# Performance work log

Measured on AMD Instinct MI355X. Metric: run time of the kernel, lower is better.

The kernel has to match this reference:

```python
import jax, jax.numpy as jnp
import numpy as np

B, T, D, H = 2, 2048, 2048, 16
HD = D // H  # 128


def _rope_tables(t, hd):
    # standard RoPE frequencies
    inv_freq = 1.0 / (10000.0 ** (np.arange(0, hd, 2, dtype=np.float32) / hd))
    pos = np.arange(t, dtype=np.float32)
    freqs = np.outer(pos, inv_freq)          # [t, hd/2]
    emb = np.concatenate([freqs, freqs], -1)  # [t, hd]
    return jnp.asarray(np.cos(emb)), jnp.asarray(np.sin(emb))


def setup_inputs() -> dict:
    key = jax.random.key(0)
    k1, k2, k3 = jax.random.split(key, 3)
    x = jax.random.normal(k1, (B, T, D), dtype=jnp.float32)
    cos, sin = _rope_tables(T, HD)
    Wqkv = jax.random.normal(k2, (3 * D, D), dtype=jnp.float32) * (D ** -0.5)
    Wout = jax.random.normal(k3, (D, D), dtype=jnp.float32) * (D ** -0.5)
    return {"x": x, "cos": cos, "sin": sin, "Wqkv": Wqkv, "Wout": Wout}


def _rotate_half(u):
    u1, u2 = jnp.split(u, 2, axis=-1)
    return jnp.concatenate([-u2, u1], axis=-1)


def _apply_rotary(u, cos, sin):
    # u: [b,h,t,hd]; cos/sin: [t,hd] broadcast over b,h
    return u * cos[None, None] + _rotate_half(u) * sin[None, None]


def reference(x, cos, sin, Wqkv, Wout):
    b, t, d = x.shape
    qkv = jnp.einsum('btd,ed->bte', x, Wqkv)                 # [b,t,3d]
    qkv = qkv.reshape(b, t, 3, H, HD).transpose(2, 0, 3, 1, 4)  # [3,b,h,t,hd]
    q, k, v = qkv[0], qkv[1], qkv[2]
    q = _apply_rotary(q, cos, sin)
    k = _apply_rotary(k, cos, sin)
    scale = 1.0 / jnp.sqrt(jnp.asarray(HD, dtype=x.dtype))
    scores = jnp.einsum('bhqe,bhke->bhqk', q, k) * scale      # [b,h,t,t]
    causal = jnp.tril(jnp.ones((t, t), dtype=bool))
    scores = jnp.where(causal[None, None], scores, jnp.asarray(-jnp.inf, dtype=scores.dtype))
    probs = jax.nn.softmax(scores, axis=-1)
    attn = jnp.einsum('bhqk,bhke->bhqe', probs, v)            # [b,h,t,hd]
    attn = attn.transpose(0, 2, 1, 3).reshape(b, t, d)
    return jnp.einsum('btd,ed->bte', attn, Wout)
```

## Files before the change

kernel.cpp:

```cpp
#include <hip/hip_runtime.h>
#include <hip/hip_bf16.h>
#include <stdint.h>

#define T_SEQ 2048
#define D_MODEL 2048
#define N_HEADS 16
#define HEAD_DIM 128

typedef __hip_bfloat16 bf16_t;
typedef __attribute__((ext_vector_type(8))) short short8;
typedef __attribute__((ext_vector_type(4))) short short4v;
typedef __attribute__((ext_vector_type(4))) float f32x4;
typedef __attribute__((ext_vector_type(16))) float f32x16;

__device__ __forceinline__ unsigned short f2bf(float x) {
  union { float f; unsigned u; } c; c.f = x;
  unsigned u = c.u;
  u += 0x7fffu + ((u >> 16) & 1u);
  return (unsigned short)(u >> 16);
}
__device__ __forceinline__ float bf2f(short v) {
  union { unsigned u; float f; } c;
  c.u = ((unsigned)(unsigned short)v) << 16;
  return c.f;
}
__device__ __forceinline__ void async16(const bf16_t* g, bf16_t* l) {
  __builtin_amdgcn_global_load_lds(
      (const __attribute__((address_space(1))) void*)g,
      (__attribute__((address_space(3))) void*)l, 16, 0, 0);
}

__global__ __launch_bounds__(256) void cvt3_kernel(
    const float* __restrict__ x, const float* __restrict__ wqkv,
    const float* __restrict__ wout,
    unsigned short* __restrict__ xb, unsigned short* __restrict__ wqkvb,
    unsigned short* __restrict__ woutb) {
  const int N1 = 4096 * 2048 / 4;
  const int N2 = 6144 * 2048 / 4;
  const int N3 = 2048 * 2048 / 4;
  const int total = N1 + N2 + N3;
  for (int i = blockIdx.x * 256 + threadIdx.x; i < total; i += gridDim.x * 256) {
    const float* src; unsigned short* dst; int j;
    if (i < N1)            { src = x;    dst = xb;    j = i; }
    else if (i < N1 + N2)  { src = wqkv; dst = wqkvb; j = i - N1; }
    else                   { src = wout; dst = woutb; j = i - N1 - N2; }
    float4 v = ((const float4*)src)[j];
    short4v o;
    o[0] = (short)f2bf(v.x); o[1] = (short)f2bf(v.y);
    o[2] = (short)f2bf(v.z); o[3] = (short)f2bf(v.w);
    ((short4v*)dst)[j] = o;
  }
}

template<int F32OUT>
__global__ __launch_bounds__(512, 4) void gemm_tp_kernel(
    const bf16_t* __restrict__ A, const bf16_t* __restrict__ Bm,
    float* __restrict__ Cf, unsigned short* __restrict__ Cb,
    int M, int N, int K, int nbn) {
  __shared__ bf16_t lds[36864];
  const int tid = threadIdx.x;
  const int w = tid >> 6, lane = tid & 63;
  const int wm = w >> 2, wn = w & 3;
  const int l15 = lane & 15, g = lane >> 4;

  const int nwg = gridDim.x;
  const int cpx = nwg >> 3;
  const int wg = (blockIdx.x & 7) * cpx + (blockIdx.x >> 3);
  const int bm0 = (wg / nbn) * 128, bn0 = (wg % nbn) * 256;

  const int sl = tid >> 3;
  const int su = (tid & 7) ^ (sl & 7);
  const int srow = (sl << 1) | (su >> 2);
  const int sc8 = su & 3;
  const bf16_t* agA = A + (size_t)(bm0 + srow) * K + sc8 * 8;
  const bf16_t* agB = Bm + (size_t)(bn0 + srow) * K + sc8 * 8;

#define STAGE(KT, SB) do {                                                    \
    bf16_t* _d = lds + (SB) * 12288 + w * 512;                                \
    async16(agA + (size_t)(KT) * 32, _d);                                     \
    async16(agB + (size_t)(KT) * 32, _d + 4096);                              \
    async16(agB + 128 * (size_t)K + (size_t)(KT) * 32, _d + 8192);            \
  } while (0)

  const int lhalf = l15 >> 1;
  const int aoff = lhalf * 64 + (((((l15 & 1) << 2) | g) ^ lhalf)) * 8;
  const bf16_t* Abase = lds + wm * 2048 + aoff;
  const bf16_t* Bbase = lds + 4096 + wn * 2048 + aoff;

  f32x4 acc[4][4];
#pragma unroll
  for (int i = 0; i < 4; ++i)
#pragma unroll
    for (int j = 0; j < 4; ++j)
#pragma unroll
      for (int e = 0; e < 4; ++e) acc[i][j][e] = 0.0f;

  STAGE(0, 0);
  STAGE(1, 1);

  const int NT = K >> 5;
  int cb = 0, sb = 2;
  for (int kt = 0; kt < NT - 1; ++kt) {
    asm volatile("s_waitcnt vmcnt(3)" ::: "memory");
    __builtin_amdgcn_s_barrier();
    const bf16_t* Ab = Abase + cb * 12288;
    const bf16_t* Bb = Bbase + cb * 12288;
    short8 af[4], bfr[4];
#pragma unroll
    for (int mi = 0; mi < 4; ++mi) af[mi] = *(const short8*)(Ab + mi * 512);
#pragma unroll
    for (int ni = 0; ni < 4; ++ni) bfr[ni] = *(const short8*)(Bb + ni * 512);
    if (kt < NT - 2) STAGE(kt + 2, sb);
    __builtin_amdgcn_s_setprio(1);
#pragma unroll
    for (int mi = 0; mi < 4; ++mi)
#pragma unroll
      for (int ni = 0; ni < 4; ++ni)
        acc[mi][ni] = __builtin_amdgcn_mfma_f32_16x16x32_bf16(
            af[mi], bfr[ni], acc[mi][ni], 0, 0, 0);
    __builtin_amdgcn_s_setprio(0);
    cb = (cb == 2) ? 0 : cb + 1;
    sb = (sb == 2) ? 0 : sb + 1;
  }
  {
    asm volatile("s_waitcnt vmcnt(0)" ::: "memory");
    __builtin_amdgcn_s_barrier();
    const bf16_t* Ab = Abase + cb * 12288;
    const bf16_t* Bb = Bbase + cb * 12288;
    short8 af[4], bfr[4];
#pragma unroll
    for (int mi = 0; mi < 4; ++mi) af[mi] = *(const short8*)(Ab + mi * 512);
#pragma unroll
    for (int ni = 0; ni < 4; ++ni) bfr[ni] = *(const short8*)(Bb + ni * 512);
    __builtin_amdgcn_s_setprio(1);
#pragma unroll
    for (int mi = 0; mi < 4; ++mi)
#pragma unroll
      for (int ni = 0; ni < 4; ++ni)
        acc[mi][ni] = __builtin_amdgcn_mfma_f32_16x16x32_bf16(
            af[mi], bfr[ni], acc[mi][ni], 0, 0, 0);
    __builtin_amdgcn_s_setprio(0);
  }
#undef STAGE

#pragma unroll
  for (int mi = 0; mi < 4; ++mi)
#pragma unroll
    for (int ni = 0; ni < 4; ++ni)
#pragma unroll
      for (int r = 0; r < 4; ++r) {
        int mr = bm0 + wm * 64 + mi * 16 + g * 4 + r;
        int nc = bn0 + wn * 64 + ni * 16 + l15;
        if (F32OUT)
          Cf[(size_t)mr * N + nc] = acc[mi][ni][r];
        else
          Cb[(size_t)mr * N + nc] = f2bf(acc[mi][ni][r]);
      }
}

__global__ __launch_bounds__(256) void rope_kernel(
    const bf16_t* __restrict__ qkv,
    const float* __restrict__ cosb, const float* __restrict__ sinb,
    bf16_t* __restrict__ qo, bf16_t* __restrict__ ko, bf16_t* __restrict__ vT) {
  const int nTT = T_SEQ / 64;
  const int bx = blockIdx.x;
  const int bh = bx / nTT, tt = bx % nTT;
  const int b = bh / N_HEADS, h = bh % N_HEADS;
  const int tid = threadIdx.x;
  __shared__ bf16_t vlds[64][136];

  const float SC = 0.08838834764831845f;

#pragma unroll
  for (int it = 0; it < 2; ++it) {
    int item = it * 256 + tid;
    int r = item >> 3, cg = item & 7;
    int t = tt * 64 + r;
    int c0 = cg * 8;
    size_t base = ((size_t)b * T_SEQ + t) * (size_t)(3 * D_MODEL) + (size_t)h * HEAD_DIM;

    float cs0[8], sn0[8], cs1[8], sn1[8];
    {
      const float* cp = cosb + (size_t)t * HEAD_DIM + c0;
      const float* sp = sinb + (size_t)t * HEAD_DIM + c0;
      float4 a0 = *(const float4*)(cp), a1 = *(const float4*)(cp + 4);
      float4 b0 = *(const float4*)(cp + 64), b1 = *(const float4*)(cp + 68);
      float4 s0 = *(const float4*)(sp), s1 = *(const float4*)(sp + 4);
      float4 t0 = *(const float4*)(sp + 64), t1 = *(const float4*)(sp + 68);
      cs0[0]=a0.x; cs0[1]=a0.y; cs0[2]=a0.z; cs0[3]=a0.w; cs0[4]=a1.x; cs0[5]=a1.y; cs0[6]=a1.z; cs0[7]=a1.w;
      cs1[0]=b0.x; cs1[1]=b0.y; cs1[2]=b0.z; cs1[3]=b0.w; cs1[4]=b1.x; cs1[5]=b1.y; cs1[6]=b1.z; cs1[7]=b1.w;
      sn0[0]=s0.x; sn0[1]=s0.y; sn0[2]=s0.z; sn0[3]=s0.w; sn0[4]=s1.x; sn0[5]=s1.y; sn0[6]=s1.z; sn0[7]=s1.w;
      sn1[0]=t0.x; sn1[1]=t0.y; sn1[2]=t0.z; sn1[3]=t0.w; sn1[4]=t1.x; sn1[5]=t1.y; sn1[6]=t1.z; sn1[7]=t1.w;
    }

#pragma unroll
    for (int sec = 0; sec < 2; ++sec) {
      size_t sbase = base + (size_t)sec * D_MODEL;
      short8 lo = *(const short8*)(qkv + sbase + c0);
      short8 hi = *(const short8*)(qkv + sbase + 64 + c0);
      short8 olo, ohi;
#pragma unroll
      for (int e = 0; e < 8; ++e) {
        float xl = bf2f(lo[e]), xh = bf2f(hi[e]);
        float rl = xl * cs0[e] - xh * sn0[e];
        float rh = xh * cs1[e] + xl * sn1[e];
        if (sec == 0) { rl *= SC; rh *= SC; }
        olo[e] = (short)f2bf(rl);
        ohi[e] = (short)f2bf(rh);
      }
      bf16_t* dst = (sec == 0 ? qo : ko) + ((size_t)bh * T_SEQ + t) * HEAD_DIM + c0;
      *(short8*)dst = olo;
      *(short8*)(dst + 64) = ohi;
    }

    short8 v0 = *(const short8*)(qkv + base + 2 * D_MODEL + c0);
    short8 v1 = *(const short8*)(qkv + base + 2 * D_MODEL + 64 + c0);
    *(short8*)&vlds[r][c0] = v0;
    *(short8*)&vlds[r][64 + c0] = v1;
  }
  __syncthreads();

  int hd = tid >> 1, hf = tid & 1;
  bf16_t* dst = vT + ((size_t)bh * HEAD_DIM + hd) * T_SEQ + tt * 64 + hf * 32;
#pragma unroll
  for (int jj = 0; jj < 4; ++jj) {
    short8 o;
#pragma unroll
    for (int e = 0; e < 8; ++e)
      o[e] = *(const short*)&vlds[hf * 32 + jj * 8 + e][hd];
    *(short8*)(dst + jj * 8) = o;
  }
}

__global__ __launch_bounds__(256, 2) void attn_kernel(
    const bf16_t* __restrict__ q, const bf16_t* __restrict__ k,
    const bf16_t* __restrict__ vT, unsigned short* __restrict__ attn) {
  const int bx = blockIdx.x;
  const int bh = bx & 31;
  const int qi = (bx >> 5) & 7;
  const int qt = (bx >> 8) ? qi : 15 - qi;
  const int b = bh / N_HEADS, h = bh % N_HEADS;
  const int tid = threadIdx.x;
  const int w = tid >> 6, lane = tid & 63;
  const int l31 = lane & 31, hi = lane >> 5;
  const int swz = l31 & 7;
  const float LOG2E = 1.44269504088896340736f;

  __shared__ bf16_t smem[32768];

  const bf16_t* qb = q + (size_t)bh * T_SEQ * HEAD_DIM;
  const bf16_t* kb = k + (size_t)bh * T_SEQ * HEAD_DIM;
  const bf16_t* vb = vT + (size_t)bh * HEAD_DIM * T_SEQ;

  const int qlo = qt * 128 + w * 32;
  const int qhi = qlo + 31;
  const int qrow = qlo + l31;

  short8 qf[8];
#pragma unroll
  for (int ks = 0; ks < 8; ++ks)
    qf[ks] = *(const short8*)(qb + (size_t)qrow * HEAD_DIM + ks * 16 + hi * 8);

  float m = -3.0e38f, l = 0.0f;
  f32x16 O[4];
#pragma unroll
  for (int dt = 0; dt < 4; ++dt)
#pragma unroll
    for (int r = 0; r < 16; ++r) O[dt][r] = 0.0f;

#define STAGE_TILES(KT, BU) {                                                    \
    _Pragma("unroll")                                                            \
    for (int j = 0; j < 4; ++j) {                                                \
      int s = j * 4 + w;                                                         \
      int row = s * 4 + (lane >> 4);                                             \
      int gc = (lane & 15) ^ (row & 7);                                          \
      async16(kb + (size_t)((KT) * 64 + row) * HEAD_DIM + gc * 8,                \
              smem + (BU) * 8192 + s * 512);                                     \
    }                                                                            \
    _Pragma("unroll")                                                            \
    for (int j = 0; j < 4; ++j) {                                                \
      int s = j * 4 + w;                                                         \
      int row = s * 8 + (lane >> 3);                                             \
      int gc = (lane & 7) ^ (row & 7);                                           \
      async16(vb + (size_t)row * T_SEQ + (KT) * 64 + gc * 8,                     \
              smem + 16384 + (BU) * 8192 + s * 512);                             \
    }                                                                            \
  }

  STAGE_TILES(0, 0);
  __syncthreads();
  int buf = 0;

  const int lastk = 2 * qt + 1;
  for (int kt = 0; kt <= lastk; ++kt) {
    if (kt < lastk) STAGE_TILES(kt + 1, buf ^ 1);
    const bf16_t* Ks = smem + buf * 8192;
    const bf16_t* Vs = smem + 16384 + buf * 8192;
    const bool active = (kt * 64 <= qhi);

    if (active) {
      f32x16 S[2];
#pragma unroll
      for (int kvt = 0; kvt < 2; ++kvt) {
        const int kvbase = kt * 64 + kvt * 32;
        if (kvbase <= qhi) {
          const int krow = kvt * 32 + l31;
#pragma unroll
          for (int r = 0; r < 16; ++r) S[kvt][r] = 0.0f;
          __builtin_amdgcn_s_setprio(1);
#pragma unroll
          for (int ks = 0; ks < 8; ++ks) {
            int c = (2 * ks + hi) ^ swz;
            short8 kf = *(const short8*)(Ks + krow * 128 + c * 8);
            S[kvt] = __builtin_amdgcn_mfma_f32_32x32x16_bf16(kf, qf[ks], S[kvt], 0, 0, 0);
          }
          __builtin_amdgcn_s_setprio(0);
          if (kvbase + 31 > qlo) {
#pragma unroll
            for (int r = 0; r < 16; ++r) {
              int kv = kvbase + (r & 3) + 8 * (r >> 2) + 4 * hi;
              if (kv > qrow) S[kvt][r] = -3.0e38f;
            }
          }
        } else {
#pragma unroll
          for (int r = 0; r < 16; ++r) S[kvt][r] = -3.0e38f;
        }
      }

      float rl = -3.0e38f;
#pragma unroll
      for (int kvt = 0; kvt < 2; ++kvt)
#pragma unroll
        for (int r = 0; r < 16; ++r) rl = fmaxf(rl, S[kvt][r]);
      rl = fmaxf(rl, __shfl_xor(rl, 32, 64));
      const bool defer = __all(rl <= m + 8.0f) != 0;
      if (!defer) {
        float mn = fmaxf(m, rl);
        float fac = exp2f((m - mn) * LOG2E);
        m = mn;
        l *= fac;
#pragma unroll
        for (int dt = 0; dt < 4; ++dt)
#pragma unroll
          for (int r = 0; r < 16; ++r) O[dt][r] *= fac;
      }
      float sum = 0.0f;
#pragma unroll
      for (int kvt = 0; kvt < 2; ++kvt)
#pragma unroll
        for (int r = 0; r < 16; ++r) {
          float p = exp2f((S[kvt][r] - m) * LOG2E);
          S[kvt][r] = p;
          sum += p;
        }
      sum += __shfl_xor(sum, 32, 64);
      l += sum;

      short8 pf[4];
#pragma unroll
      for (int ks = 0; ks < 4; ++ks) {
        const int kvt = ks >> 1;
        const int base = (ks & 1) * 8;
        unsigned pkL0, pkL1, pkH0, pkH1;
        {
          float a0 = S[kvt][base + 0], a1 = S[kvt][base + 1];
          float a2 = S[kvt][base + 2], a3 = S[kvt][base + 3];
          float b0 = S[kvt][base + 4], b1 = S[kvt][base + 5];
          float b2 = S[kvt][base + 6], b3 = S[kvt][base + 7];
          asm("v_cvt_pk_bf16_f32 %0, %1, %2" : "=v"(pkL0) : "v"(a0), "v"(a1));
          asm("v_cvt_pk_bf16_f32 %0, %1, %2" : "=v"(pkL1) : "v"(a2), "v"(a3));
          asm("v_cvt_pk_bf16_f32 %0, %1, %2" : "=v"(pkH0) : "v"(b0), "v"(b1));
          asm("v_cvt_pk_bf16_f32 %0, %1, %2" : "=v"(pkH1) : "v"(b2), "v"(b3));
        }
        unsigned sx0 = hi ? pkL0 : pkH0;
        unsigned sx1 = hi ? pkL1 : pkH1;
        unsigned rx0 = (unsigned)__shfl_xor((int)sx0, 32, 64);
        unsigned rx1 = (unsigned)__shfl_xor((int)sx1, 32, 64);
        union { unsigned u[4]; short8 s; } uu;
        uu.u[0] = hi ? rx0 : pkL0;
        uu.u[1] = hi ? rx1 : pkL1;
        uu.u[2] = hi ? pkH0 : rx0;
        uu.u[3] = hi ? pkH1 : rx1;
        pf[ks] = uu.s;
      }

      __builtin_amdgcn_s_setprio(1);
#pragma unroll
      for (int dt = 0; dt < 4; ++dt) {
        const int vrow = dt * 32 + l31;
#pragma unroll
        for (int ks = 0; ks < 4; ++ks) {
          int c = (2 * ks + hi) ^ swz;
          short8 vf = *(const short8*)(Vs + vrow * 64 + c * 8);
          O[dt] = __builtin_amdgcn_mfma_f32_32x32x16_bf16(vf, pf[ks], O[dt], 0, 0, 0);
        }
      }
      __builtin_amdgcn_s_setprio(0);
    }

    __syncthreads();
    buf ^= 1;
  }
#undef STAGE_TILES

  float inv = 1.0f / l;
  bf16_t* ol = smem + w * 4352;
#pragma unroll
  for (int dt = 0; dt < 4; ++dt)
#pragma unroll
    for (int r = 0; r < 16; ++r) {
      int d = dt * 32 + (r & 3) + 8 * (r >> 2) + 4 * hi;
      *(unsigned short*)&ol[l31 * 136 + d] = f2bf(O[dt][r] * inv);
    }
  __syncthreads();
  const int srow4 = lane >> 4;
  const int scol = (lane & 15) * 8;
#pragma unroll
  for (int rr = 0; rr < 8; ++rr) {
    int row = rr * 4 + srow4;
    short8 v = *(const short8*)(ol + row * 136 + scol);
    *(short8*)(attn + ((size_t)b * T_SEQ + qt * 128 + w * 32 + row) * D_MODEL +
               (size_t)h * HEAD_DIM + scol) = v;
  }
}

extern "C" void kernel_launch(void* const* d_in, const int* in_sizes, int n_in,
                              void* d_out, int out_size, void* d_ws, size_t ws_size,
                              hipStream_t stream) {
  const float* x    = (const float*)d_in[0];
  const float* cosb = (const float*)d_in[1];
  const float* sinb = (const float*)d_in[2];
  const float* Wqkv = (const float*)d_in[3];
  const float* Wout = (const float*)d_in[4];
  float* out = (float*)d_out;

  char* ws = (char*)d_ws;
  size_t off = 0;
  bf16_t* xb    = (bf16_t*)(ws + off); off += (size_t)4096 * 2048 * 2;
  bf16_t* wqkvb = (bf16_t*)(ws + off); off += (size_t)6144 * 2048 * 2;
  bf16_t* woutb = (bf16_t*)(ws + off); off += (size_t)2048 * 2048 * 2;
  bf16_t* qkvb  = (bf16_t*)(ws + off); off += (size_t)4096 * 6144 * 2;
  bf16_t* qb    = (bf16_t*)(ws + off); off += (size_t)32 * 2048 * 128 * 2;
  bf16_t* kb    = (bf16_t*)(ws + off); off += (size_t)32 * 2048 * 128 * 2;
  bf16_t* vTb   = (bf16_t*)(ws + off); off += (size_t)32 * 2048 * 128 * 2;
  bf16_t* attnb = xb;

  cvt3_kernel<<<2048, 256, 0, stream>>>(x, Wqkv, Wout,
                                        (unsigned short*)xb, (unsigned short*)wqkvb,
                                        (unsigned short*)woutb);

  gemm_tp_kernel<0><<<768, 512, 0, stream>>>(xb, wqkvb, nullptr, (unsigned short*)qkvb,
                                             4096, 6144, 2048, 24);

  rope_kernel<<<1024, 256, 0, stream>>>(qkvb, cosb, sinb, qb, kb, vTb);

  attn_kernel<<<512, 256, 0, stream>>>(qb, kb, vTb, (unsigned short*)attnb);

  gemm_tp_kernel<1><<<256, 512, 0, stream>>>(attnb, woutb, out, nullptr,
                                             4096, 2048, 2048, 8);
}
```

Measured before the change: 263.6 us.

## Fuse RoPE, scaling and V transpose into QKV GEMM epilogue

The QKV projection GEMM epilogue now stages the output tile in LDS, then applies rotary embedding and the query scale, and writes q/k in head-major layout, or writes V transposed, directly. This removes the separate rope kernel launch and the round trip of the full bf16 qkv buffer through global memory. In exchange the GEMM epilogue does more work, with extra LDS traffic, barriers and cos/sin loads, which could raise register pressure at the current launch bounds.

```diff
diff --git a/kernel.cpp b/kernel.cpp
--- a/kernel.cpp
+++ b/kernel.cpp
@@ -52,10 +52,12 @@
   }
 }
 
-template<int F32OUT>
+template<int MODE>
 __global__ __launch_bounds__(512, 4) void gemm_tp_kernel(
     const bf16_t* __restrict__ A, const bf16_t* __restrict__ Bm,
-    float* __restrict__ Cf, unsigned short* __restrict__ Cb,
+    float* __restrict__ Cf,
+    const float* __restrict__ cosb, const float* __restrict__ sinb,
+    bf16_t* __restrict__ qo, bf16_t* __restrict__ ko, bf16_t* __restrict__ vT,
     int M, int N, int K, int nbn) {
   __shared__ bf16_t lds[36864];
   const int tid = threadIdx.x;
@@ -143,92 +145,92 @@
   }
 #undef STAGE
 
-#pragma unroll
-  for (int mi = 0; mi < 4; ++mi)
-#pragma unroll
-    for (int ni = 0; ni < 4; ++ni)
-#pragma unroll
-      for (int r = 0; r < 4; ++r) {
-        int mr = bm0 + wm * 64 + mi * 16 + g * 4 + r;
-        int nc = bn0 + wn * 64 + ni * 16 + l15;
-        if (F32OUT)
+  if (MODE == 0) {
+#pragma unroll
+    for (int mi = 0; mi < 4; ++mi)
+#pragma unroll
+      for (int ni = 0; ni < 4; ++ni)
+#pragma unroll
+        for (int r = 0; r < 4; ++r) {
+          int mr = bm0 + wm * 64 + mi * 16 + g * 4 + r;
+          int nc = bn0 + wn * 64 + ni * 16 + l15;
           Cf[(size_t)mr * N + nc] = acc[mi][ni][r];
-        else
-          Cb[(size_t)mr * N + nc] = f2bf(acc[mi][ni][r]);
-      }
-}
-
-__global__ __launch_bounds__(256) void rope_kernel(
-    const bf16_t* __restrict__ qkv,
-    const float* __restrict__ cosb, const float* __restrict__ sinb,
-    bf16_t* __restrict__ qo, bf16_t* __restrict__ ko, bf16_t* __restrict__ vT) {
-  const int nTT = T_SEQ / 64;
-  const int bx = blockIdx.x;
-  const int bh = bx / nTT, tt = bx % nTT;
-  const int b = bh / N_HEADS, h = bh % N_HEADS;
-  const int tid = threadIdx.x;
-  __shared__ bf16_t vlds[64][136];
-
-  const float SC = 0.08838834764831845f;
-
-#pragma unroll
-  for (int it = 0; it < 2; ++it) {
-    int item = it * 256 + tid;
-    int r = item >> 3, cg = item & 7;
-    int t = tt * 64 + r;
-    int c0 = cg * 8;
-    size_t base = ((size_t)b * T_SEQ + t) * (size_t)(3 * D_MODEL) + (size_t)h * HEAD_DIM;
-
-    float cs0[8], sn0[8], cs1[8], sn1[8];
-    {
-      const float* cp = cosb + (size_t)t * HEAD_DIM + c0;
-      const float* sp = sinb + (size_t)t * HEAD_DIM + c0;
-      float4 a0 = *(const float4*)(cp), a1 = *(const float4*)(cp + 4);
-      float4 b0 = *(const float4*)(cp + 64), b1 = *(const float4*)(cp + 68);
-      float4 s0 = *(const float4*)(sp), s1 = *(const float4*)(sp + 4);
-      float4 t0 = *(const float4*)(sp + 64), t1 = *(const float4*)(sp + 68);
-      cs0[0]=a0.x; cs0[1]=a0.y; cs0[2]=a0.z; cs0[3]=a0.w; cs0[4]=a1.x; cs0[5]=a1.y; cs0[6]=a1.z; cs0[7]=a1.w;
-      cs1[0]=b0.x; cs1[1]=b0.y; cs1[2]=b0.z; cs1[3]=b0.w; cs1[4]=b1.x; cs1[5]=b1.y; cs1[6]=b1.z; cs1[7]=b1.w;
-      sn0[0]=s0.x; sn0[1]=s0.y; sn0[2]=s0.z; sn0[3]=s0.w; sn0[4]=s1.x; sn0[5]=s1.y; sn0[6]=s1.z; sn0[7]=s1.w;
-      sn1[0]=t0.x; sn1[1]=t0.y; sn1[2]=t0.z; sn1[3]=t0.w; sn1[4]=t1.x; sn1[5]=t1.y; sn1[6]=t1.z; sn1[7]=t1.w;
+        }
+    return;
+  }
+
+  const int region = bn0 >> 11;
+  const int bb = bm0 >> 11;
+  const int t0 = bm0 & 2047;
+  __syncthreads();
+
+  if (region < 2) {
+#pragma unroll
+    for (int mi = 0; mi < 4; ++mi)
+#pragma unroll
+      for (int ni = 0; ni < 4; ++ni)
+#pragma unroll
+        for (int r = 0; r < 4; ++r) {
+          int lr = wm * 64 + mi * 16 + g * 4 + r;
+          int lc = wn * 64 + ni * 16 + l15;
+          *(unsigned short*)&lds[lr * 264 + lc] = f2bf(acc[mi][ni][r]);
+        }
+    __syncthreads();
+
+    const float SC = (region == 0) ? 0.08838834764831845f : 1.0f;
+    bf16_t* outp = (region == 0) ? qo : ko;
+#pragma unroll
+    for (int it = 0; it < 8; ++it) {
+      int item = it * 512 + tid;
+      int row = item >> 5;
+      int col = (item & 31) * 8;
+      int cg = (bn0 & 2047) + col;
+      int h = cg >> 7, hd = cg & 127;
+      int t = t0 + row;
+      short8 u  = *(const short8*)&lds[row * 264 + col];
+      short8 up = *(const short8*)&lds[row * 264 + ((hd & 64) ? col - 64 : col + 64)];
+      const float* cp = cosb + (size_t)t * HEAD_DIM + hd;
+      const float* sp = sinb + (size_t)t * HEAD_DIM + hd;
+      float4 c0 = *(const float4*)cp, c1 = *(const float4*)(cp + 4);
+      float4 s0 = *(const float4*)sp, s1 = *(const float4*)(sp + 4);
+      float cs[8] = {c0.x, c0.y, c0.z, c0.w, c1.x, c1.y, c1.z, c1.w};
+      float sn[8] = {s0.x, s0.y, s0.z, s0.w, s1.x, s1.y, s1.z, s1.w};
+      short8 o;
+#pragma unroll
+      for (int e = 0; e < 8; ++e) {
+        float xl = bf2f(u[e]), xp = bf2f(up[e]);
+        float res = (hd & 64) ? (xl * cs[e] + xp * sn[e])
+                              : (xl * cs[e] - xp * sn[e]);
+        o[e] = (short)f2bf(res * SC);
+      }
+      *(short8*)(outp + ((size_t)(bb * 16 + h) * T_SEQ + t) * HEAD_DIM + hd) = o;
     }
-
-#pragma unroll
-    for (int sec = 0; sec < 2; ++sec) {
-      size_t sbase = base + (size_t)sec * D_MODEL;
-      short8 lo = *(const short8*)(qkv + sbase + c0);
-      short8 hi = *(const short8*)(qkv + sbase + 64 + c0);
-      short8 olo, ohi;
-#pragma unroll
-      for (int e = 0; e < 8; ++e) {
-        float xl = bf2f(lo[e]), xh = bf2f(hi[e]);
-        float rl = xl * cs0[e] - xh * sn0[e];
-        float rh = xh * cs1[e] + xl * sn1[e];
-        if (sec == 0) { rl *= SC; rh *= SC; }
-        olo[e] = (short)f2bf(rl);
-        ohi[e] = (short)f2bf(rh);
-      }
-      bf16_t* dst = (sec == 0 ? qo : ko) + ((size_t)bh * T_SEQ + t) * HEAD_DIM + c0;
-      *(short8*)dst = olo;
-      *(short8*)(dst + 64) = ohi;
+  } else {
+#pragma unroll
+    for (int mi = 0; mi < 4; ++mi)
+#pragma unroll
+      for (int ni = 0; ni < 4; ++ni) {
+        int lc = wn * 64 + ni * 16 + l15;
+        int lr = wm * 64 + mi * 16 + g * 4;
+        short4v p;
+        p[0] = (short)f2bf(acc[mi][ni][0]);
+        p[1] = (short)f2bf(acc[mi][ni][1]);
+        p[2] = (short)f2bf(acc[mi][ni][2]);
+        p[3] = (short)f2bf(acc[mi][ni][3]);
+        *(short4v*)&lds[lc * 136 + lr] = p;
+      }
+    __syncthreads();
+
+#pragma unroll
+    for (int it = 0; it < 8; ++it) {
+      int item = it * 512 + tid;
+      int col = item >> 4;
+      int tch = (item & 15) * 8;
+      short8 v = *(const short8*)&lds[col * 136 + tch];
+      int cg = (bn0 & 2047) + col;
+      int h = cg >> 7, hd = cg & 127;
+      *(short8*)(vT + ((size_t)(bb * 16 + h) * HEAD_DIM + hd) * T_SEQ + t0 + tch) = v;
     }
-
-    short8 v0 = *(const short8*)(qkv + base + 2 * D_MODEL + c0);
-    short8 v1 = *(const short8*)(qkv + base + 2 * D_MODEL + 64 + c0);
-    *(short8*)&vlds[r][c0] = v0;
-    *(short8*)&vlds[r][64 + c0] = v1;
-  }
-  __syncthreads();
-
-  int hd = tid >> 1, hf = tid & 1;
-  bf16_t* dst = vT + ((size_t)bh * HEAD_DIM + hd) * T_SEQ + tt * 64 + hf * 32;
-#pragma unroll
-  for (int jj = 0; jj < 4; ++jj) {
-    short8 o;
-#pragma unroll
-    for (int e = 0; e < 8; ++e)
-      o[e] = *(const short*)&vlds[hf * 32 + jj * 8 + e][hd];
-    *(short8*)(dst + jj * 8) = o;
   }
 }
 
@@ -440,7 +442,6 @@
   bf16_t* xb    = (bf16_t*)(ws + off); off += (size_t)4096 * 2048 * 2;
   bf16_t* wqkvb = (bf16_t*)(ws + off); off += (size_t)6144 * 2048 * 2;
   bf16_t* woutb = (bf16_t*)(ws + off); off += (size_t)2048 * 2048 * 2;
-  bf16_t* qkvb  = (bf16_t*)(ws + off); off += (size_t)4096 * 6144 * 2;
   bf16_t* qb    = (bf16_t*)(ws + off); off += (size_t)32 * 2048 * 128 * 2;
   bf16_t* kb    = (bf16_t*)(ws + off); off += (size_t)32 * 2048 * 128 * 2;
   bf16_t* vTb   = (bf16_t*)(ws + off); off += (size_t)32 * 2048 * 128 * 2;
@@ -450,13 +451,12 @@
                                         (unsigned short*)xb, (unsigned short*)wqkvb,
                                         (unsigned short*)woutb);
 
-  gemm_tp_kernel<0><<<768, 512, 0, stream>>>(xb, wqkvb, nullptr, (unsigned short*)qkvb,
-                                             4096, 6144, 2048, 24);
-
-  rope_kernel<<<1024, 256, 0, stream>>>(qkvb, cosb, sinb, qb, kb, vTb);
+  gemm_tp_kernel<1><<<768, 512, 0, stream>>>(xb, wqkvb, nullptr, cosb, sinb,
+                                             qb, kb, vTb, 4096, 6144, 2048, 24);
 
   attn_kernel<<<512, 256, 0, stream>>>(qb, kb, vTb, (unsigned short*)attnb);
 
-  gemm_tp_kernel<1><<<256, 512, 0, stream>>>(attnb, woutb, out, nullptr,
+  gemm_tp_kernel<0><<<256, 512, 0, stream>>>(attnb, woutb, out, nullptr, nullptr,
+                                             nullptr, nullptr, nullptr,
                                              4096, 2048, 2048, 8);
 }
```

Result: faster. 242.8 us (-7.9%).
